# Optimization experiments

Hardware: AMD Instinct MI355X
Metric: run time of the kernel (lower is better)

The kernel has to match this reference:

```python
import jax, jax.numpy as jnp
import numpy as np
from jax import lax

N, E = 100000, 1600000
IN_DIM, EDGE_DIM, HIDDEN, LAYERS, HEADS, OUT_DIM = 16, 4, 128, 6, 8, 3
C = HIDDEN // HEADS  # per-head dim
EPS = 1e-5


def setup_inputs() -> dict:
    key = jax.random.key(0)
    ks = jax.random.split(key, 24)
    s = 0.1
    inp = {
        "x": jax.random.normal(ks[0], (N, IN_DIM), jnp.float32),
        "edge_index": jax.random.randint(ks[1], (2, E), 0, N, jnp.int32),
        "edge_attr": jax.random.normal(ks[2], (E, EDGE_DIM), jnp.float32),
        # input projection
        "W_in": s * jax.random.normal(ks[3], (IN_DIM, HIDDEN), jnp.float32),
        "b_in": jnp.zeros((HIDDEN,), jnp.float32),
        "ln_in_g": jnp.ones((HIDDEN,), jnp.float32),
        "ln_in_b": jnp.zeros((HIDDEN,), jnp.float32),
        # stacked GAT layer params [L, ...]
        "Wg": s * jax.random.normal(ks[4], (LAYERS, HIDDEN, HIDDEN), jnp.float32),
        "att_src": s * jax.random.normal(ks[5], (LAYERS, HEADS, C), jnp.float32),
        "att_dst": s * jax.random.normal(ks[6], (LAYERS, HEADS, C), jnp.float32),
        "We": s * jax.random.normal(ks[7], (LAYERS, EDGE_DIM, HIDDEN), jnp.float32),
        "att_edge": s * jax.random.normal(ks[8], (LAYERS, HEADS, C), jnp.float32),
        "bg": jnp.zeros((LAYERS, HIDDEN), jnp.float32),
        "ln_g": jnp.ones((LAYERS, HIDDEN), jnp.float32),
        "ln_b": jnp.zeros((LAYERS, HIDDEN), jnp.float32),
        # output head
        "W1": s * jax.random.normal(ks[9], (HIDDEN, HIDDEN), jnp.float32),
        "b1": jnp.zeros((HIDDEN,), jnp.float32),
        "W2": s * jax.random.normal(ks[10], (HIDDEN, OUT_DIM), jnp.float32),
        "b2": jnp.zeros((OUT_DIM,), jnp.float32),
    }
    return inp


def layer_norm(x, g, b):
    mu = jnp.mean(x, axis=-1, keepdims=True)
    var = jnp.var(x, axis=-1, keepdims=True)
    return (x - mu) * lax.rsqrt(var + EPS) * g + b


def gat_block(h, src, dst, edge_attr, Wg, a_s, a_d, We, a_e, bg, g, b):
    # linear projection, shared for src/dst (same input set in PyG GATConv)
    hp = (h @ Wg).reshape(N, HEADS, C)                  # [N,H,C]
    alpha_src = jnp.sum(hp * a_s, axis=-1)              # [N,H]
    alpha_dst = jnp.sum(hp * a_d, axis=-1)              # [N,H]
    ep = (edge_attr @ We).reshape(E, HEADS, C)          # [E,H,C]
    alpha_e = jnp.sum(ep * a_e, axis=-1)                # [E,H]
    # edge-wise attention logits, leaky_relu slope 0.2 (PyG default)
    alpha = jax.nn.leaky_relu(alpha_src[src] + alpha_dst[dst] + alpha_e, 0.2)
    # segment softmax over incoming edges of each dst node
    m = jax.ops.segment_max(alpha, dst, num_segments=N)  # [N,H]
    m = jnp.where(jnp.isfinite(m), m, 0.0)
    a = jnp.exp(alpha - m[dst])
    denom = jax.ops.segment_sum(a, dst, num_segments=N)  # [N,H]
    a = a / (denom[dst] + 1e-16)
    # weighted message aggregation
    msg = hp[src] * a[:, :, None]                        # [E,H,C]
    out = jax.ops.segment_sum(msg, dst, num_segments=N).reshape(N, HIDDEN) + bg
    # residual + LayerNorm (dropout inactive in eval)
    return layer_norm(h + out, g, b)


def reference(x, edge_index, edge_attr, W_in, b_in, ln_in_g, ln_in_b,
              Wg, att_src, att_dst, We, att_edge, bg, ln_g, ln_b,
              W1, b1, W2, b2):
    src, dst = edge_index[0], edge_index[1]
    h = layer_norm(jax.nn.relu(x @ W_in + b_in), ln_in_g, ln_in_b)

    def body(h, p):
        Wg_i, as_i, ad_i, We_i, ae_i, bg_i, g_i, b_i = p
        return gat_block(h, src, dst, edge_attr, Wg_i, as_i, ad_i, We_i, ae_i, bg_i, g_i, b_i), None

    h, _ = lax.scan(body, h, (Wg, att_src, att_dst, We, att_edge, bg, ln_g, ln_b))
    h = jax.nn.relu(h @ W1 + b1)
    return jax.nn.relu(h @ W2 + b2)
```

## Files before the change

### kernel.cpp

```cpp
#include <hip/hip_runtime.h>
#include <hip/hip_bf16.h>

#define NN 100000
#define NE 1600000
#define HID 128
#define NH 8
#define HC 16
#define NL 6
#define CAP 64

typedef unsigned int u32;

__device__ __forceinline__ float u2f(unsigned short v){
  union{u32 i; float f;} c; c.i = ((u32)v) << 16; return c.f;
}
__device__ __forceinline__ float lo2f(u32 u){ union{u32 i; float f;} c; c.i = u << 16; return c.f; }
__device__ __forceinline__ float hi2f(u32 u){ union{u32 i; float f;} c; c.i = u & 0xFFFF0000u; return c.f; }
__device__ __forceinline__ unsigned short f2bf(float f){
  u32 u = __float_as_uint(f);
  u = (u + 0x7FFFu + ((u >> 16) & 1u)) >> 16;
  return (unsigned short)u;
}

__device__ __forceinline__ float ldw(const void* p, long long i, int fl){
  if (fl) return ((const float*)p)[i];
  return u2f(((const unsigned short*)p)[i]);
}

__global__ void sniff_k(const void* g, int* flag){
  if (threadIdx.x == 0 && blockIdx.x == 0){
    const unsigned short* p = (const unsigned short*)g;
    flag[0] = (p[0] == 0x3F80) ? 0 : 1;
  }
}

__global__ void zero_k(int* p, int n){
  int i = blockIdx.x*256 + threadIdx.x;
  if (i < n) p[i] = 0;
}

#define PF_TOT 4355
__global__ void prep_params_k(const void* att_src, const void* att_dst,
    const void* bg, const void* ln_g, const void* ln_b, const void* b1,
    const void* W2, const void* b2, float* __restrict__ pf, const int* flag){
  int fl = flag[0];
  int i = blockIdx.x*256 + threadIdx.x;
  if (i >= PF_TOT) return;
  float v;
  if (i < 768)       v = ldw(att_src, i, fl);
  else if (i < 1536) v = ldw(att_dst, i-768, fl);
  else if (i < 2304) v = ldw(bg, i-1536, fl);
  else if (i < 3072) v = ldw(ln_g, i-2304, fl);
  else if (i < 3840) v = ldw(ln_b, i-3072, fl);
  else if (i < 3968) v = ldw(b1, i-3840, fl);
  else if (i < 4352) v = ldw(W2, i-3968, fl);
  else               v = ldw(b2, i-4352, fl);
  pf[i] = v;
}

__global__ __launch_bounds__(256) void prep_wf_k(const void* Wg, const void* W1,
    float* __restrict__ wF, const int* flag){
  int fl = flag[0];
  long long i = (long long)blockIdx.x*256 + threadIdx.x;
  if (i >= (long long)7*HID*HID) return;
  float v = (i < (long long)6*HID*HID) ? ldw(Wg, i, fl) : ldw(W1, i - (long long)6*HID*HID, fl);
  wF[i] = v;
}

__global__ void prep_wae_k(const void* We, const void* ae, float* __restrict__ Wae,
                           const int* flag){
  int fl = flag[0];
  int id = threadIdx.x;
  if (id >= NL*4*NH) return;
  int l = id / 32, r = id % 32, d = r / 8, hh = r % 8;
  float s = 0.f;
  #pragma unroll
  for (int c = 0; c < HC; ++c)
    s += ldw(We, l*4*HID + d*HID + hh*HC + c, fl) * ldw(ae, l*NH*HC + hh*HC + c, fl);
  Wae[id] = s;
}

__global__ __launch_bounds__(256) void inproj_k(const void* x,
    const void* W_in, const void* b_in, const void* g, const void* b,
    float* __restrict__ h, const int* flag){
  __shared__ float xs[2][16];
  __shared__ float r1[2][2], r2[2][2];
  int fl = flag[0];
  int half = threadIdx.x >> 7;
  int t = threadIdx.x & 127;
  long long n = (long long)blockIdx.x*2 + half;
  if (t < 16) xs[half][t] = ldw(x, n*16 + t, fl);
  __syncthreads();
  float acc = ldw(b_in, t, fl);
  #pragma unroll
  for (int k = 0; k < 16; ++k) acc = fmaf(xs[half][k], ldw(W_in, k*HID + t, fl), acc);
  acc = fmaxf(acc, 0.f);
  float s1 = acc, s2 = acc*acc;
  #pragma unroll
  for (int off = 32; off; off >>= 1){ s1 += __shfl_xor(s1, off); s2 += __shfl_xor(s2, off); }
  if ((t & 63) == 0){ r1[half][t>>6] = s1; r2[half][t>>6] = s2; }
  __syncthreads();
  float S1 = r1[half][0] + r1[half][1], S2 = r2[half][0] + r2[half][1];
  float mu = S1 * (1.f/128.f);
  float var = S2 * (1.f/128.f) - mu*mu;
  float rr = rsqrtf(var + 1e-5f);
  h[n*HID + t] = (acc - mu) * rr * ldw(g, t, fl) + ldw(b, t, fl);
}

__global__ __launch_bounds__(256) void count_k(const int* __restrict__ dst,
    int* __restrict__ deg, int* __restrict__ pos){
  int e = blockIdx.x*256 + threadIdx.x;
  if (e >= NE) return;
  pos[e] = atomicAdd(&deg[dst[e]], 1);
}
__global__ __launch_bounds__(256) void scan_block_k(const int* __restrict__ in,
    int* __restrict__ out, int* __restrict__ bsum, int n){
  __shared__ int lds[256];
  int t = threadIdx.x, i = blockIdx.x*256 + t;
  int v = (i < n) ? in[i] : 0;
  lds[t] = v;
  __syncthreads();
  #pragma unroll
  for (int off = 1; off < 256; off <<= 1){
    int tmp = (t >= off) ? lds[t-off] : 0;
    __syncthreads();
    lds[t] += tmp;
    __syncthreads();
  }
  int incl = lds[t];
  if (i < n) out[i] = incl - v;
  if (t == 255) bsum[blockIdx.x] = incl;
}
__global__ __launch_bounds__(512) void scan_top_k(const int* __restrict__ bsum,
    int* __restrict__ boff, int nb){
  __shared__ int lds[512];
  int t = threadIdx.x;
  int v = (t < nb) ? bsum[t] : 0;
  lds[t] = v;
  __syncthreads();
  #pragma unroll
  for (int off = 1; off < 512; off <<= 1){
    int tmp = (t >= off) ? lds[t-off] : 0;
    __syncthreads();
    lds[t] += tmp;
    __syncthreads();
  }
  boff[t] = lds[t] - v;
}
__global__ __launch_bounds__(256) void scan_add_k(int* __restrict__ rowptr,
    const int* __restrict__ boff, int n){
  int i = blockIdx.x*256 + threadIdx.x;
  if (i < n) rowptr[i] += boff[i >> 8];
  if (i == 0) rowptr[n] = NE;
}
__global__ __launch_bounds__(256) void scatter_k(const int* __restrict__ src,
    const int* __restrict__ dst, const int* __restrict__ rowptr,
    const int* __restrict__ pos, const void* eattr,
    uint4* __restrict__ pk, const int* flag){
  int fl = flag[0];
  int e = blockIdx.x*256 + threadIdx.x;
  if (e >= NE) return;
  int d = dst[e];
  int i = rowptr[d] + pos[e];
  uint4 o;
  o.x = (u32)src[e];
  if (fl){
    float4 v = *(const float4*)((const float*)eattr + (long long)e*4);
    o.y = ((u32)f2bf(v.y) << 16) | (u32)f2bf(v.x);
    o.z = ((u32)f2bf(v.w) << 16) | (u32)f2bf(v.z);
  } else {
    uint2 er = *(const uint2*)((const unsigned short*)eattr + (long long)e*4);
    o.y = er.x; o.z = er.y;
  }
  o.w = 0;
  pk[i] = o;
}

__global__ __launch_bounds__(256) void gemm128_k(const float* __restrict__ A,
    const float* __restrict__ WF, unsigned short* __restrict__ Cout,
    const float* __restrict__ biasF, int relu,
    const float* __restrict__ attS, const float* __restrict__ attD,
    float* __restrict__ asrc, float* __restrict__ adst){
  __shared__ float At[32][132];
  __shared__ float Wt[32][132];
  int t = threadIdx.x;
  int row0 = blockIdx.x * 128;
  int tx = t & 15, ty = t >> 4;
  float acc[8][8] = {};
  for (int k0 = 0; k0 < 128; k0 += 32){
    int ar = t >> 1, ak = (t & 1) * 16;
    float a16[16];
    int arow = row0 + ar;
    if (arow < NN){
      const float* ap = A + (long long)arow*HID + k0 + ak;
      float4 q0 = *(const float4*)ap, q1 = *(const float4*)(ap+4);
      float4 q2 = *(const float4*)(ap+8), q3 = *(const float4*)(ap+12);
      a16[0]=q0.x; a16[1]=q0.y; a16[2]=q0.z; a16[3]=q0.w;
      a16[4]=q1.x; a16[5]=q1.y; a16[6]=q1.z; a16[7]=q1.w;
      a16[8]=q2.x; a16[9]=q2.y; a16[10]=q2.z; a16[11]=q2.w;
      a16[12]=q3.x; a16[13]=q3.y; a16[14]=q3.z; a16[15]=q3.w;
    } else {
      #pragma unroll
      for (int j = 0; j < 16; ++j) a16[j] = 0.f;
    }
    int wk = t >> 3, wn = (t & 7) * 16;
    float w16[16];
    {
      const float* wp = WF + (long long)(k0 + wk)*HID + wn;
      float4 q0 = *(const float4*)wp, q1 = *(const float4*)(wp+4);
      float4 q2 = *(const float4*)(wp+8), q3 = *(const float4*)(wp+12);
      w16[0]=q0.x; w16[1]=q0.y; w16[2]=q0.z; w16[3]=q0.w;
      w16[4]=q1.x; w16[5]=q1.y; w16[6]=q1.z; w16[7]=q1.w;
      w16[8]=q2.x; w16[9]=q2.y; w16[10]=q2.z; w16[11]=q2.w;
      w16[12]=q3.x; w16[13]=q3.y; w16[14]=q3.z; w16[15]=q3.w;
    }
    __syncthreads();
    #pragma unroll
    for (int j = 0; j < 16; ++j) At[ak+j][ar] = a16[j];
    #pragma unroll
    for (int j = 0; j < 16; j += 4){
      float4 q; q.x=w16[j]; q.y=w16[j+1]; q.z=w16[j+2]; q.w=w16[j+3];
      *(float4*)&Wt[wk][wn+j] = q;
    }
    __syncthreads();
    #pragma unroll
    for (int kk = 0; kk < 32; ++kk){
      float4 a0 = *(const float4*)&At[kk][ty*8];
      float4 a1 = *(const float4*)&At[kk][ty*8+4];
      float4 b0 = *(const float4*)&Wt[kk][tx*4];
      float4 b1 = *(const float4*)&Wt[kk][64 + tx*4];
      float am[8] = {a0.x,a0.y,a0.z,a0.w,a1.x,a1.y,a1.z,a1.w};
      float bn[8] = {b0.x,b0.y,b0.z,b0.w,b1.x,b1.y,b1.z,b1.w};
      #pragma unroll
      for (int i2 = 0; i2 < 8; ++i2){
        #pragma unroll
        for (int j2 = 0; j2 < 8; ++j2)
          acc[i2][j2] = fmaf(am[i2], bn[j2], acc[i2][j2]);
      }
    }
  }
  float bb[8];
  #pragma unroll
  for (int j2 = 0; j2 < 8; ++j2){
    int col = (j2 < 4) ? tx*4 + j2 : 64 + tx*4 + (j2 - 4);
    bb[j2] = biasF ? biasF[col] : 0.f;
  }
  #pragma unroll
  for (int i2 = 0; i2 < 8; ++i2){
    int row = row0 + ty*8 + i2;
    if (row < NN){
      float o[8];
      #pragma unroll
      for (int j2 = 0; j2 < 8; ++j2){
        float v = acc[i2][j2] + bb[j2];
        o[j2] = relu ? fmaxf(v, 0.f) : v;
      }
      uint2 p0, p1;
      p0.x = ((u32)f2bf(o[1]) << 16) | (u32)f2bf(o[0]);
      p0.y = ((u32)f2bf(o[3]) << 16) | (u32)f2bf(o[2]);
      p1.x = ((u32)f2bf(o[5]) << 16) | (u32)f2bf(o[4]);
      p1.y = ((u32)f2bf(o[7]) << 16) | (u32)f2bf(o[6]);
      *(uint2*)(Cout + (long long)row*HID + tx*4) = p0;
      *(uint2*)(Cout + (long long)row*HID + 64 + tx*4) = p1;
    }
  }
  if (attS){
    float (*pas)[8][4] = (float (*)[8][4])&At[0][0];
    float (*pad)[8][4] = (float (*)[8][4])&Wt[0][0];
    float avS[8], avD[8];
    #pragma unroll
    for (int j2 = 0; j2 < 8; ++j2){
      int col = (j2 < 4) ? tx*4 + j2 : 64 + tx*4 + (j2 - 4);
      avS[j2] = attS[col]; avD[j2] = attD[col];
    }
    int h0 = tx >> 2, slot = tx & 3;
    __syncthreads();
    #pragma unroll
    for (int i2 = 0; i2 < 8; ++i2){
      float ps0 = 0.f, pd0 = 0.f, ps1 = 0.f, pd1 = 0.f;
      #pragma unroll
      for (int j2 = 0; j2 < 4; ++j2){
        ps0 = fmaf(acc[i2][j2],   avS[j2],   ps0);
        pd0 = fmaf(acc[i2][j2],   avD[j2],   pd0);
        ps1 = fmaf(acc[i2][j2+4], avS[j2+4], ps1);
        pd1 = fmaf(acc[i2][j2+4], avD[j2+4], pd1);
      }
      int row = ty*8 + i2;
      pas[row][h0][slot] = ps0;   pad[row][h0][slot] = pd0;
      pas[row][h0+4][slot] = ps1; pad[row][h0+4][slot] = pd1;
    }
    __syncthreads();
    #pragma unroll
    for (int q = 0; q < 4; ++q){
      int idx = t + 256*q;
      int row = idx >> 3, hh = idx & 7;
      int rr = row0 + row;
      if (rr < NN){
        asrc[(long long)rr*NH + hh] = pas[row][hh][0] + pas[row][hh][1]
                                    + pas[row][hh][2] + pas[row][hh][3];
        adst[(long long)rr*NH + hh] = pad[row][hh][0] + pad[row][hh][1]
                                    + pad[row][hh][2] + pad[row][hh][3];
      }
    }
  }
}

__global__ __launch_bounds__(256) void gat_node_k(const int* __restrict__ rowptr,
    const uint4* __restrict__ pk,
    const float* __restrict__ Wae_l, const float* __restrict__ asrc,
    const float* __restrict__ adst, const unsigned short* __restrict__ hp,
    float* __restrict__ h, const float* __restrict__ bgF,
    const float* __restrict__ gF, const float* __restrict__ bF){
  __shared__ float lw[4][CAP][8];
  __shared__ int   ls[4][CAP];
  int wv = threadIdx.x >> 6, l = threadIdx.x & 63;
  int n = blockIdx.x*4 + wv;
  int b0 = rowptr[n], b1 = rowptr[n+1];
  int deg = b1 - b0;
  int sub = l >> 3, hh = l & 7;
  float wae0 = Wae_l[hh], wae1 = Wae_l[8+hh], wae2 = Wae_l[16+hh], wae3 = Wae_l[24+hh];
  float adn = adst[n*NH + hh];
  float den = 0.f;
  for (int i = b0 + sub; i < b1; i += 8){
    uint4 q = pk[i];
    int s = (int)q.x;
    float v = asrc[s*NH + hh] + adn;
    v = fmaf(lo2f(q.y), wae0, v);
    v = fmaf(hi2f(q.y), wae1, v);
    v = fmaf(lo2f(q.z), wae2, v);
    v = fmaf(hi2f(q.z), wae3, v);
    v = fmaxf(v, 0.2f*v);
    float w = __expf(v);
    int idx = i - b0;
    if (idx < CAP){
      lw[wv][idx][hh] = w;
      if (hh == 0) ls[wv][idx] = s;
    }
    den += w;
  }
  den += __shfl_xor(den, 8);
  den += __shfl_xor(den, 16);
  den += __shfl_xor(den, 32);
  int eg = l >> 4, cl = l & 15;
  int hd = cl >> 1;
  float rden = 1.f / (__shfl(den, hd) + 1e-16f);
  const unsigned short* hpc = hp + 8*cl;
  float a[8] = {0,0,0,0,0,0,0,0};
  int cap_end = b0 + (deg < CAP ? deg : CAP);
  int i = b0;
  for (; i + 8 <= cap_end; i += 8){
    int j0 = i + eg, j1 = i + 4 + eg;
    int s0 = ls[wv][j0 - b0], s1v = ls[wv][j1 - b0];
    float w0 = lw[wv][j0 - b0][hd], w1 = lw[wv][j1 - b0][hd];
    uint4 q0 = *(const uint4*)(hpc + (long long)s0*HID);
    uint4 q1 = *(const uint4*)(hpc + (long long)s1v*HID);
    a[0] = fmaf(w0, lo2f(q0.x), a[0]); a[1] = fmaf(w0, hi2f(q0.x), a[1]);
    a[2] = fmaf(w0, lo2f(q0.y), a[2]); a[3] = fmaf(w0, hi2f(q0.y), a[3]);
    a[4] = fmaf(w0, lo2f(q0.z), a[4]); a[5] = fmaf(w0, hi2f(q0.z), a[5]);
    a[6] = fmaf(w0, lo2f(q0.w), a[6]); a[7] = fmaf(w0, hi2f(q0.w), a[7]);
    a[0] = fmaf(w1, lo2f(q1.x), a[0]); a[1] = fmaf(w1, hi2f(q1.x), a[1]);
    a[2] = fmaf(w1, lo2f(q1.y), a[2]); a[3] = fmaf(w1, hi2f(q1.y), a[3]);
    a[4] = fmaf(w1, lo2f(q1.z), a[4]); a[5] = fmaf(w1, hi2f(q1.z), a[5]);
    a[6] = fmaf(w1, lo2f(q1.w), a[6]); a[7] = fmaf(w1, hi2f(q1.w), a[7]);
  }
  for (; i < cap_end; i += 4){
    int j = i + eg;
    if (j < cap_end){
      int s = ls[wv][j - b0];
      float w = lw[wv][j - b0][hd];
      uint4 q = *(const uint4*)(hpc + (long long)s*HID);
      a[0] = fmaf(w, lo2f(q.x), a[0]); a[1] = fmaf(w, hi2f(q.x), a[1]);
      a[2] = fmaf(w, lo2f(q.y), a[2]); a[3] = fmaf(w, hi2f(q.y), a[3]);
      a[4] = fmaf(w, lo2f(q.z), a[4]); a[5] = fmaf(w, hi2f(q.z), a[5]);
      a[6] = fmaf(w, lo2f(q.w), a[6]); a[7] = fmaf(w, hi2f(q.w), a[7]);
    }
  }
  if (deg > CAP){
    float w0c = Wae_l[hd], w1c = Wae_l[8+hd], w2c = Wae_l[16+hd], w3c = Wae_l[24+hd];
    float adc = adst[n*NH + hd];
    for (int j = cap_end + eg; j < b1; j += 4){
      uint4 e4 = pk[j];
      int s = (int)e4.x;
      float v = asrc[s*NH + hd] + adc;
      v = fmaf(lo2f(e4.y), w0c, v);
      v = fmaf(hi2f(e4.y), w1c, v);
      v = fmaf(lo2f(e4.z), w2c, v);
      v = fmaf(hi2f(e4.z), w3c, v);
      v = fmaxf(v, 0.2f*v);
      float w = __expf(v);
      uint4 q = *(const uint4*)(hpc + (long long)s*HID);
      a[0] = fmaf(w, lo2f(q.x), a[0]); a[1] = fmaf(w, hi2f(q.x), a[1]);
      a[2] = fmaf(w, lo2f(q.y), a[2]); a[3] = fmaf(w, hi2f(q.y), a[3]);
      a[4] = fmaf(w, lo2f(q.z), a[4]); a[5] = fmaf(w, hi2f(q.z), a[5]);
      a[6] = fmaf(w, lo2f(q.w), a[6]); a[7] = fmaf(w, hi2f(q.w), a[7]);
    }
  }
  #pragma unroll
  for (int j = 0; j < 8; ++j){
    a[j] += __shfl_xor(a[j], 16);
    a[j] += __shfl_xor(a[j], 32);
  }
  const float* hrow = h + (long long)n*HID + 8*cl;
  float4 hv0 = *(const float4*)hrow;
  float4 hv1 = *(const float4*)(hrow + 4);
  float hv[8] = {hv0.x,hv0.y,hv0.z,hv0.w,hv1.x,hv1.y,hv1.z,hv1.w};
  float tv[8];
  float s1 = 0.f, s2 = 0.f;
  #pragma unroll
  for (int j = 0; j < 8; ++j){
    tv[j] = hv[j] + a[j]*rden + bgF[8*cl + j];
    s1 += tv[j]; s2 += tv[j]*tv[j];
  }
  s1 += __shfl_xor(s1, 1); s2 += __shfl_xor(s2, 1);
  s1 += __shfl_xor(s1, 2); s2 += __shfl_xor(s2, 2);
  s1 += __shfl_xor(s1, 4); s2 += __shfl_xor(s2, 4);
  s1 += __shfl_xor(s1, 8); s2 += __shfl_xor(s2, 8);
  float mu = s1 * (1.f/128.f);
  float var = s2 * (1.f/128.f) - mu*mu;
  float rr = rsqrtf(var + 1e-5f);
  if (eg == 0){
    float4 o0, o1;
    o0.x = (tv[0]-mu)*rr*gF[8*cl+0] + bF[8*cl+0];
    o0.y = (tv[1]-mu)*rr*gF[8*cl+1] + bF[8*cl+1];
    o0.z = (tv[2]-mu)*rr*gF[8*cl+2] + bF[8*cl+2];
    o0.w = (tv[3]-mu)*rr*gF[8*cl+3] + bF[8*cl+3];
    o1.x = (tv[4]-mu)*rr*gF[8*cl+4] + bF[8*cl+4];
    o1.y = (tv[5]-mu)*rr*gF[8*cl+5] + bF[8*cl+5];
    o1.z = (tv[6]-mu)*rr*gF[8*cl+6] + bF[8*cl+6];
    o1.w = (tv[7]-mu)*rr*gF[8*cl+7] + bF[8*cl+7];
    *(float4*)(h + (long long)n*HID + 8*cl) = o0;
    *(float4*)(h + (long long)n*HID + 8*cl + 4) = o1;
  }
}

__global__ __launch_bounds__(256) void head2_k(const unsigned short* __restrict__ hp,
    const float* __restrict__ W2F, const float* __restrict__ b2F, void* out,
    const int* flag){
  int fl = flag[0];
  int n = blockIdx.x*4 + (threadIdx.x >> 6);
  if (n >= NN) return;
  int l = threadIdx.x & 63;
  u32 u = *(const u32*)(hp + (long long)n*HID + 2*l);
  float p0 = lo2f(u), p1 = hi2f(u);
  int c0 = 2*l, c1 = 2*l + 1;
  float o0 = p0*W2F[c0*3+0] + p1*W2F[c1*3+0];
  float o1 = p0*W2F[c0*3+1] + p1*W2F[c1*3+1];
  float o2 = p0*W2F[c0*3+2] + p1*W2F[c1*3+2];
  #pragma unroll
  for (int off = 32; off; off >>= 1){
    o0 += __shfl_xor(o0, off); o1 += __shfl_xor(o1, off); o2 += __shfl_xor(o2, off);
  }
  if (l == 0){
    float r0 = fmaxf(o0 + b2F[0], 0.f);
    float r1 = fmaxf(o1 + b2F[1], 0.f);
    float r2 = fmaxf(o2 + b2F[2], 0.f);
    if (fl){
      float* o = (float*)out;
      o[n*3+0] = r0; o[n*3+1] = r1; o[n*3+2] = r2;
    } else {
      unsigned short* o = (unsigned short*)out;
      o[n*3+0] = f2bf(r0); o[n*3+1] = f2bf(r1); o[n*3+2] = f2bf(r2);
    }
  }
}

extern "C" void kernel_launch(void* const* d_in, const int* in_sizes, int n_in,
                              void* d_out, int out_size, void* d_ws, size_t ws_size,
                              hipStream_t stream){
  const void* x       = d_in[0];
  const int*  eidx    = (const int*)d_in[1];
  const void* eattr   = d_in[2];
  const void* W_in    = d_in[3];
  const void* b_in    = d_in[4];
  const void* ln_in_g = d_in[5];
  const void* ln_in_b = d_in[6];
  const void* Wg      = d_in[7];
  const void* att_src = d_in[8];
  const void* att_dst = d_in[9];
  const void* We      = d_in[10];
  const void* att_e   = d_in[11];
  const void* bg      = d_in[12];
  const void* ln_g    = d_in[13];
  const void* ln_b    = d_in[14];
  const void* W1      = d_in[15];
  const void* b1v     = d_in[16];
  const void* W2      = d_in[17];
  const void* b2      = d_in[18];

  char* ws = (char*)d_ws;
  size_t off = 0;
  auto alloc = [&](size_t bytes) -> void* {
    void* p = ws + off; off += (bytes + 255) & ~(size_t)255; return p;
  };
  float*  h     = (float*) alloc((size_t)NN*HID*4);
  unsigned short* hp = (unsigned short*)alloc((size_t)NN*HID*2);
  float*  asrc  = (float*) alloc((size_t)NN*NH*4);
  float*  adst  = (float*) alloc((size_t)NN*NH*4);
  float*  Wae   = (float*) alloc(NL*32*4);
  float*  pf    = (float*) alloc(PF_TOT*4);
  float*  wF    = (float*) alloc((size_t)7*HID*HID*4);
  int* deg      = (int*)   alloc((size_t)NN*4);
  int* pos      = (int*)   alloc((size_t)NE*4);
  int* rowptr   = (int*)   alloc((size_t)(NN+1)*4);
  int* bsum     = (int*)   alloc(512*4);
  int* boffp    = (int*)   alloc(512*4);
  uint4* pk     = (uint4*) alloc((size_t)NE*16);
  int* flag     = (int*)   alloc(256);

  const int* src = eidx;
  const int* dst = eidx + NE;
  int nb = (NN + 255) / 256;

  sniff_k<<<1, 64, 0, stream>>>(ln_in_g, flag);
  zero_k<<<nb, 256, 0, stream>>>(deg, NN);
  prep_wae_k<<<1, 256, 0, stream>>>(We, att_e, Wae, flag);
  prep_params_k<<<(PF_TOT+255)/256, 256, 0, stream>>>(att_src, att_dst, bg, ln_g, ln_b,
                                                      b1v, W2, b2, pf, flag);
  prep_wf_k<<<(7*HID*HID+255)/256, 256, 0, stream>>>(Wg, W1, wF, flag);
  inproj_k<<<NN/2, 256, 0, stream>>>(x, W_in, b_in, ln_in_g, ln_in_b, h, flag);
  count_k<<<(NE+255)/256, 256, 0, stream>>>(dst, deg, pos);
  scan_block_k<<<nb, 256, 0, stream>>>(deg, rowptr, bsum, NN);
  scan_top_k<<<1, 512, 0, stream>>>(bsum, boffp, nb);
  scan_add_k<<<nb, 256, 0, stream>>>(rowptr, boffp, NN);
  scatter_k<<<(NE+255)/256, 256, 0, stream>>>(src, dst, rowptr, pos, eattr, pk, flag);

  const float* attS = pf;
  const float* attD = pf + 768;
  const float* bgF  = pf + 1536;
  const float* gF   = pf + 2304;
  const float* bF   = pf + 3072;
  const float* b1F  = pf + 3840;
  const float* W2F  = pf + 3968;
  const float* b2F  = pf + 4352;

  int gblocks = (NN + 127) / 128;
  for (int l = 0; l < NL; ++l){
    gemm128_k<<<gblocks, 256, 0, stream>>>(h, wF + (size_t)l*HID*HID, hp,
                                           nullptr, 0, attS + l*128, attD + l*128,
                                           asrc, adst);
    gat_node_k<<<NN/4, 256, 0, stream>>>(rowptr, pk, Wae + l*32, asrc, adst,
                                         hp, h, bgF + l*128, gF + l*128, bF + l*128);
  }
  gemm128_k<<<gblocks, 256, 0, stream>>>(h, wF + (size_t)6*HID*HID, hp, b1F, 1,
                                         nullptr, nullptr, nullptr, nullptr);
  head2_k<<<(NN+3)/4, 256, 0, stream>>>(hp, W2F, b2F, d_out, flag);
}
```

Baseline: 1.280 ms.

## Double-buffer GEMM shared tiles and store A tile as bf16

The 128-wide GEMM kernel now double-buffers its shared-memory A and W tiles. The next K-slice is staged while the current one is computed, which removes one barrier per iteration. The A tile is converted to bf16 in shared memory, cutting LDS footprint and read width, at the cost of rounding A before the multiply and extra conversion work. The attention-score scratch pointers are remapped to the new buffers; pad now aliases the smaller bf16 At buffer, which may overlap incorrectly if it needs more than 8.7KB.

```diff
diff --git a/kernel.cpp b/kernel.cpp
--- a/kernel.cpp
+++ b/kernel.cpp
@@ -181,55 +181,55 @@
     const float* __restrict__ biasF, int relu,
     const float* __restrict__ attS, const float* __restrict__ attD,
     float* __restrict__ asrc, float* __restrict__ adst){
-  __shared__ float At[32][132];
-  __shared__ float Wt[32][132];
+  __shared__ unsigned short At[2][32][136];
+  __shared__ float Wt[2][32][132];
   int t = threadIdx.x;
   int row0 = blockIdx.x * 128;
   int tx = t & 15, ty = t >> 4;
-  float acc[8][8] = {};
-  for (int k0 = 0; k0 < 128; k0 += 32){
-    int ar = t >> 1, ak = (t & 1) * 16;
-    float a16[16];
-    int arow = row0 + ar;
-    if (arow < NN){
+  int ar = t >> 1, ak = (t & 1) * 16;
+  int wk = t >> 3, wn = (t & 7) * 16;
+  int arow = row0 + ar;
+  int avalid = arow < NN;
+
+  auto stage = [&](int k0, int buf){
+    unsigned short a16[16];
+    if (avalid){
       const float* ap = A + (long long)arow*HID + k0 + ak;
       float4 q0 = *(const float4*)ap, q1 = *(const float4*)(ap+4);
       float4 q2 = *(const float4*)(ap+8), q3 = *(const float4*)(ap+12);
-      a16[0]=q0.x; a16[1]=q0.y; a16[2]=q0.z; a16[3]=q0.w;
-      a16[4]=q1.x; a16[5]=q1.y; a16[6]=q1.z; a16[7]=q1.w;
-      a16[8]=q2.x; a16[9]=q2.y; a16[10]=q2.z; a16[11]=q2.w;
-      a16[12]=q3.x; a16[13]=q3.y; a16[14]=q3.z; a16[15]=q3.w;
+      a16[0]=f2bf(q0.x); a16[1]=f2bf(q0.y); a16[2]=f2bf(q0.z); a16[3]=f2bf(q0.w);
+      a16[4]=f2bf(q1.x); a16[5]=f2bf(q1.y); a16[6]=f2bf(q1.z); a16[7]=f2bf(q1.w);
+      a16[8]=f2bf(q2.x); a16[9]=f2bf(q2.y); a16[10]=f2bf(q2.z); a16[11]=f2bf(q2.w);
+      a16[12]=f2bf(q3.x); a16[13]=f2bf(q3.y); a16[14]=f2bf(q3.z); a16[15]=f2bf(q3.w);
     } else {
       #pragma unroll
-      for (int j = 0; j < 16; ++j) a16[j] = 0.f;
-    }
-    int wk = t >> 3, wn = (t & 7) * 16;
-    float w16[16];
-    {
-      const float* wp = WF + (long long)(k0 + wk)*HID + wn;
-      float4 q0 = *(const float4*)wp, q1 = *(const float4*)(wp+4);
-      float4 q2 = *(const float4*)(wp+8), q3 = *(const float4*)(wp+12);
-      w16[0]=q0.x; w16[1]=q0.y; w16[2]=q0.z; w16[3]=q0.w;
-      w16[4]=q1.x; w16[5]=q1.y; w16[6]=q1.z; w16[7]=q1.w;
-      w16[8]=q2.x; w16[9]=q2.y; w16[10]=q2.z; w16[11]=q2.w;
-      w16[12]=q3.x; w16[13]=q3.y; w16[14]=q3.z; w16[15]=q3.w;
-    }
-    __syncthreads();
+      for (int j = 0; j < 16; ++j) a16[j] = 0;
+    }
     #pragma unroll
-    for (int j = 0; j < 16; ++j) At[ak+j][ar] = a16[j];
-    #pragma unroll
-    for (int j = 0; j < 16; j += 4){
-      float4 q; q.x=w16[j]; q.y=w16[j+1]; q.z=w16[j+2]; q.w=w16[j+3];
-      *(float4*)&Wt[wk][wn+j] = q;
-    }
-    __syncthreads();
+    for (int j = 0; j < 16; ++j) At[buf][ak+j][ar] = a16[j];
+    const float* wp = WF + (long long)(k0 + wk)*HID + wn;
+    float4 q0 = *(const float4*)wp, q1 = *(const float4*)(wp+4);
+    float4 q2 = *(const float4*)(wp+8), q3 = *(const float4*)(wp+12);
+    *(float4*)&Wt[buf][wk][wn]    = q0;
+    *(float4*)&Wt[buf][wk][wn+4]  = q1;
+    *(float4*)&Wt[buf][wk][wn+8]  = q2;
+    *(float4*)&Wt[buf][wk][wn+12] = q3;
+  };
+
+  float acc[8][8] = {};
+  stage(0, 0);
+  __syncthreads();
+  #pragma unroll
+  for (int it = 0; it < 4; ++it){
+    int cur = it & 1;
+    if (it < 3) stage((it + 1) * 32, cur ^ 1);
     #pragma unroll
     for (int kk = 0; kk < 32; ++kk){
-      float4 a0 = *(const float4*)&At[kk][ty*8];
-      float4 a1 = *(const float4*)&At[kk][ty*8+4];
-      float4 b0 = *(const float4*)&Wt[kk][tx*4];
-      float4 b1 = *(const float4*)&Wt[kk][64 + tx*4];
-      float am[8] = {a0.x,a0.y,a0.z,a0.w,a1.x,a1.y,a1.z,a1.w};
+      uint4 au = *(const uint4*)&At[cur][kk][ty*8];
+      float4 b0 = *(const float4*)&Wt[cur][kk][tx*4];
+      float4 b1 = *(const float4*)&Wt[cur][kk][64 + tx*4];
+      float am[8] = {lo2f(au.x), hi2f(au.x), lo2f(au.y), hi2f(au.y),
+                     lo2f(au.z), hi2f(au.z), lo2f(au.w), hi2f(au.w)};
       float bn[8] = {b0.x,b0.y,b0.z,b0.w,b1.x,b1.y,b1.z,b1.w};
       #pragma unroll
       for (int i2 = 0; i2 < 8; ++i2){
@@ -238,6 +238,7 @@
           acc[i2][j2] = fmaf(am[i2], bn[j2], acc[i2][j2]);
       }
     }
+    __syncthreads();
   }
   float bb[8];
   #pragma unroll
@@ -265,8 +266,8 @@
     }
   }
   if (attS){
-    float (*pas)[8][4] = (float (*)[8][4])&At[0][0];
-    float (*pad)[8][4] = (float (*)[8][4])&Wt[0][0];
+    float (*pas)[8][4] = (float (*)[8][4])&Wt[0][0][0];
+    float (*pad)[8][4] = (float (*)[8][4])&At[0][0][0];
     float avS[8], avD[8];
     #pragma unroll
     for (int j2 = 0; j2 < 8; ++j2){
```

New measurement: 1.524 ms. +19.0%, slower.
